# Performance work log

Hardware: AMD Instinct MI355X
Metric: run time of the kernel (lower is better)

## Reference

```python
import jax, jax.numpy as jnp
import numpy as np
import math

EMBED_DIM = 64

def setup_inputs() -> dict:
    key = jax.random.key(0)
    ks = jax.random.split(key, 9)
    B, S, H, E = 2, 2048, 8, EMBED_DIM
    f16 = jnp.float16
    inp = {
        'query': jax.random.normal(ks[0], (B, S, H, E), dtype=f16),
        'key':   jax.random.normal(ks[1], (B, S, H, E), dtype=f16),
        'value': jax.random.normal(ks[2], (B, S, H, E), dtype=f16),
        # Linear params (torch Linear: y = x @ W.T + b); W stored as [out,in]
        'Wq': (jax.random.normal(ks[3], (E, E), dtype=f16) / np.float16(math.sqrt(E))),
        'bq': jax.random.normal(ks[4], (E,), dtype=f16) * np.float16(0.02),
        'Wk': (jax.random.normal(ks[5], (E, E), dtype=f16) / np.float16(math.sqrt(E))),
        'bk': jax.random.normal(ks[6], (E,), dtype=f16) * np.float16(0.02),
        'Wv': (jax.random.normal(ks[7], (E, E), dtype=f16) / np.float16(math.sqrt(E))),
        'bv': jax.random.normal(ks[8], (E,), dtype=f16) * np.float16(0.02),
    }
    return inp

def reference(query, key, value, Wq, bq, Wk, bk, Wv, bv):
    # Linear projections on last dim, fused with permute(0,2,1,3): [B,S,H,E] -> [B,H,S,E]
    q = jnp.einsum('bshe,fe->bhsf', query, Wq) + bq
    k = jnp.einsum('bshe,fe->bhsf', key, Wk) + bk
    v = jnp.einsum('bshe,fe->bhsf', value, Wv) + bv
    scale = jnp.asarray(1.0 / math.sqrt(q.shape[-1]), dtype=q.dtype)
    q = q * scale
    # full attention matrix [B,H,S,S], fp16 matmul then fp32 softmax (faithful to source)
    scores = jnp.einsum('bhse,bhte->bhst', q, k).astype(jnp.float32)
    attn = jax.nn.softmax(scores, axis=-1).astype(jnp.float16)
    out = jnp.einsum('bhst,bhte->bhse', attn, v)
    return out
```

## Files before the change

### kernel.cpp

```cpp
#include <hip/hip_runtime.h>

#define S_LEN 2048
#define NH    8
#define EMB   64
#define BM    64
#define BN    64
#define NKT   (S_LEN / BN)
#define NSPLIT 2
#define M_INIT  (-1.0e4f)
#define EXP_CLAMP (-80.0f)
#define DEFER_THR 8.0f

typedef _Float16 half8   __attribute__((ext_vector_type(8)));
typedef _Float16 half4   __attribute__((ext_vector_type(4)));
typedef float    float4_t __attribute__((ext_vector_type(4)));
typedef float    float8_t __attribute__((ext_vector_type(8)));

__device__ inline half8 cvt8(const float* p) {
    float8_t f = *reinterpret_cast<const float8_t*>(p);
    half8 h;
    #pragma unroll
    for (int j = 0; j < 8; ++j) h[j] = (_Float16)f[j];
    return h;
}

__device__ inline void gload_lds16(const _Float16* g, _Float16* l) {
    __builtin_amdgcn_global_load_lds(
        (const __attribute__((address_space(1))) void*)g,
        (__attribute__((address_space(3))) void*)l, 16, 0, 0);
}

__device__ inline void proj_body(
    int mode, int bid, const float* __restrict__ X,
    const float* __restrict__ W, const float* __restrict__ bias,
    _Float16* __restrict__ Dst)
{
    const int tid  = threadIdx.x;
    const int lane = tid & 63;
    const int wave = tid >> 6;
    const int l15  = lane & 15;
    const int quad = lane >> 4;
    const int gwave = bid * 4 + wave;

    half8 wf[4][2];
    #pragma unroll
    for (int ft = 0; ft < 4; ++ft)
        #pragma unroll
        for (int ks = 0; ks < 2; ++ks)
            wf[ft][ks] = cvt8(W + (ft * 16 + l15) * 64 + ks * 32 + quad * 8);
    float bv[4];
    #pragma unroll
    for (int ft = 0; ft < 4; ++ft) bv[ft] = bias[ft * 16 + l15];

    #pragma unroll
    for (int rt2 = 0; rt2 < 2; ++rt2) {
        const int rt = gwave * 2 + rt2;
        const int arow = rt * 16 + l15;
        half8 xf[2];
        #pragma unroll
        for (int ks = 0; ks < 2; ++ks)
            xf[ks] = cvt8(X + (long)arow * 64 + ks * 32 + quad * 8);
        float4_t acc[4];
        #pragma unroll
        for (int ft = 0; ft < 4; ++ft) {
            acc[ft] = (float4_t){0.f, 0.f, 0.f, 0.f};
            #pragma unroll
            for (int ks = 0; ks < 2; ++ks)
                acc[ft] = __builtin_amdgcn_mfma_f32_16x16x32_f16(
                    xf[ks], wf[ft][ks], acc[ft], 0, 0, 0);
        }
        #pragma unroll
        for (int r = 0; r < 4; ++r) {
            const int row = rt * 16 + quad * 4 + r;
            const int b = row >> 14;
            const int s = (row >> 3) & 2047;
            const int h = row & 7;
            const int bh = b * NH + h;
            #pragma unroll
            for (int ft = 0; ft < 4; ++ft) {
                const _Float16 v = (_Float16)(acc[ft][r] + bv[ft]);
                const int f = ft * 16 + l15;
                if (mode == 0)
                    Dst[((long)bh * S_LEN + s) * EMB + f] = v * (_Float16)0.125f;
                else if (mode == 1)
                    Dst[(((long)bh * 8 + (f >> 3)) * S_LEN + s) * 8 + (f & 7)] = v;
                else
                    Dst[(((long)bh * 256 + (s >> 3)) * 64 + f) * 8 + (s & 7)] = v;
            }
        }
    }
}

__global__ __launch_bounds__(256) void proj_qkv(
    const float* __restrict__ q_in, const float* __restrict__ k_in,
    const float* __restrict__ v_in,
    const float* __restrict__ Wq, const float* __restrict__ bq,
    const float* __restrict__ Wk, const float* __restrict__ bk,
    const float* __restrict__ Wv, const float* __restrict__ bv_,
    _Float16* __restrict__ Qf16, _Float16* __restrict__ KT8,
    _Float16* __restrict__ VT8)
{
    const int seg = blockIdx.x >> 8;
    const int bid = blockIdx.x & 255;
    if (seg == 0)      proj_body(0, bid, q_in, Wq, bq, Qf16);
    else if (seg == 1) proj_body(1, bid, k_in, Wk, bk, KT8);
    else               proj_body(2, bid, v_in, Wv, bv_, VT8);
}

__global__ __launch_bounds__(256) void proj_qk(
    const float* __restrict__ q_in, const float* __restrict__ k_in,
    const float* __restrict__ Wq, const float* __restrict__ bq,
    const float* __restrict__ Wk, const float* __restrict__ bk,
    _Float16* __restrict__ Qf16, _Float16* __restrict__ KT8)
{
    const int seg = blockIdx.x >> 8;
    const int bid = blockIdx.x & 255;
    if (seg == 0) proj_body(0, bid, q_in, Wq, bq, Qf16);
    else          proj_body(1, bid, k_in, Wk, bk, KT8);
}

__global__ __launch_bounds__(256) void proj_v(
    const float* __restrict__ v_in,
    const float* __restrict__ Wv, const float* __restrict__ bv_,
    _Float16* __restrict__ VT8)
{
    proj_body(2, blockIdx.x, v_in, Wv, bv_, VT8);
}

__global__ __launch_bounds__(512, 4) void attn_fused(
    const _Float16* __restrict__ KT, const _Float16* __restrict__ VT,
    const _Float16* __restrict__ Qf16, float* __restrict__ out)
{
    extern __shared__ __align__(16) char smem[];
    _Float16* KV = (_Float16*)smem;

    const int tid  = threadIdx.x;
    const int lane = tid & 63;
    const int wave = tid >> 6;
    const int g    = wave >> 2;
    const int w4   = wave & 3;
    const int l15  = lane & 15;
    const int quad = lane >> 4;
    const int tid_g = tid & 255;

    _Float16* Kb0 = KV + (g * 4 + 0) * 4096;
    _Float16* Kb1 = KV + (g * 4 + 1) * 4096;
    _Float16* Vb0 = KV + (g * 4 + 2) * 4096;
    _Float16* Vb1 = KV + (g * 4 + 3) * 4096;
    _Float16* Pw  = (_Float16*)(smem + 65536) + wave * 1024;
    float*    mrgO  = (float*)(smem + 32768);
    float*    mrgML = (float*)(smem + 49152);

    const int bx  = blockIdx.x;
    const int xcd = bx & 7;
    const int j   = bx >> 3;
    const int hh  = j >> 5;
    const int qt  = j & 31;
    const int bh  = xcd * 2 + hh;

    const int qrow0 = qt * BM + w4 * 16;
    const _Float16* kg  = KT + (long)bh * 8 * S_LEN * 8;
    const _Float16* vgh = VT + (long)bh * 256 * 512;

    const _Float16* k0 = kg + ((long)(tid_g >> 6) * S_LEN + (tid_g & 63)) * 8;
    const _Float16* k1 = kg + ((long)((tid_g >> 6) + 4) * S_LEN + (tid_g & 63)) * 8;
    const _Float16* v0 = vgh + tid_g * 8;
    const _Float16* v1 = vgh + (256 + tid_g) * 8;

    const int kb = g * (NKT / NSPLIT);

    {
        const long t8  = (long)(kb * BN) * 8;
        const long t64 = (long)(kb * BN) * 64;
        gload_lds16(k0 + t8,  Kb0 + tid_g * 8);
        gload_lds16(k1 + t8,  Kb0 + (256 + tid_g) * 8);
        gload_lds16(v0 + t64, Vb0 + tid_g * 8);
        gload_lds16(v1 + t64, Vb0 + (256 + tid_g) * 8);
    }

    half8 qf[2];
    {
        const _Float16* qrow = Qf16 + ((long)bh * S_LEN + qrow0 + l15) * EMB;
        qf[0] = *reinterpret_cast<const half8*>(qrow + quad * 8);
        qf[1] = *reinterpret_cast<const half8*>(qrow + 32 + quad * 8);
    }

    half8 vones;
    #pragma unroll
    for (int jj = 0; jj < 8; ++jj) vones[jj] = (_Float16)1.0f;

    float4_t o[4];
    #pragma unroll
    for (int et = 0; et < 4; ++et) o[et] = (float4_t){0.f, 0.f, 0.f, 0.f};
    float4_t lacc = (float4_t){0.f, 0.f, 0.f, 0.f};
    float m_run = M_INIT;

    const int pswz = (l15 & 7) << 3;
    __syncthreads();

    for (int it = 0; it < NKT / NSPLIT; ++it) {
        const int cur = it & 1;
        const bool more = (it + 1 < NKT / NSPLIT);

        if (more) {
            const long t8  = (long)((kb + it + 1) * BN) * 8;
            const long t64 = (long)((kb + it + 1) * BN) * 64;
            _Float16* kd = cur ? Kb0 : Kb1;
            _Float16* vd = cur ? Vb0 : Vb1;
            gload_lds16(k0 + t8,  kd + tid_g * 8);
            gload_lds16(k1 + t8,  kd + (256 + tid_g) * 8);
            gload_lds16(v0 + t64, vd + tid_g * 8);
            gload_lds16(v1 + t64, vd + (256 + tid_g) * 8);
        }

        const _Float16* Kc = cur ? Kb1 : Kb0;
        const _Float16* Vc = cur ? Vb1 : Vb0;

        float4_t sacc[4];
        #pragma unroll
        for (int nt = 0; nt < 4; ++nt) sacc[nt] = (float4_t){0.f, 0.f, 0.f, 0.f};
        __builtin_amdgcn_s_setprio(1);
        #pragma unroll
        for (int nt = 0; nt < 4; ++nt)
            #pragma unroll
            for (int ks = 0; ks < 2; ++ks) {
                half8 kf = *reinterpret_cast<const half8*>(
                    Kc + (ks * 4 + quad) * 512 + (nt * 16 + l15) * 8);
                sacc[nt] = __builtin_amdgcn_mfma_f32_16x16x32_f16(
                    kf, qf[ks], sacc[nt], 0, 0, 0);
            }
        __builtin_amdgcn_s_setprio(0);

        float mx = fmaxf(fmaxf(sacc[0][0], sacc[0][1]),
                         fmaxf(sacc[0][2], sacc[0][3]));
        mx = fmaxf(fmaxf(mx, sacc[1][0]), sacc[1][1]);
        mx = fmaxf(fmaxf(mx, sacc[1][2]), sacc[1][3]);
        mx = fmaxf(fmaxf(mx, sacc[2][0]), sacc[2][1]);
        mx = fmaxf(fmaxf(mx, sacc[2][2]), sacc[2][3]);
        mx = fmaxf(fmaxf(mx, sacc[3][0]), sacc[3][1]);
        mx = fmaxf(fmaxf(mx, sacc[3][2]), sacc[3][3]);

        if (!__all(mx - m_run <= DEFER_THR)) {
            float mr = fmaxf(mx, __shfl_xor(mx, 16));
            mr = fmaxf(mr, __shfl_xor(mr, 32));
            const float mn = fmaxf(m_run, mr);
            const float alpha = __expf(fmaxf(m_run - mn, EXP_CLAMP));
            m_run = mn;
            #pragma unroll
            for (int r = 0; r < 4; ++r) {
                const float ar = __shfl(alpha, quad * 4 + r);
                lacc[r] *= ar;
                #pragma unroll
                for (int et = 0; et < 4; ++et) o[et][r] *= ar;
            }
        }

        #pragma unroll
        for (int nt = 0; nt < 4; ++nt) {
            half4 ph;
            #pragma unroll
            for (int r = 0; r < 4; ++r)
                ph[r] = (_Float16)__expf(sacc[nt][r] - m_run);
            *reinterpret_cast<half4*>(
                &Pw[l15 * 64 + ((nt * 16 + quad * 4) ^ pswz)]) = ph;
        }
        half8 pf0 = *reinterpret_cast<const half8*>(
            &Pw[l15 * 64 + ((quad * 8) ^ pswz)]);
        half8 pf1 = *reinterpret_cast<const half8*>(
            &Pw[l15 * 64 + ((32 + quad * 8) ^ pswz)]);

        __builtin_amdgcn_s_setprio(1);
        #pragma unroll
        for (int et = 0; et < 4; ++et) {
            half8 vf = *reinterpret_cast<const half8*>(
                Vc + quad * 512 + (et * 16 + l15) * 8);
            o[et] = __builtin_amdgcn_mfma_f32_16x16x32_f16(pf0, vf, o[et], 0, 0, 0);
        }
        lacc = __builtin_amdgcn_mfma_f32_16x16x32_f16(pf0, vones, lacc, 0, 0, 0);
        #pragma unroll
        for (int et = 0; et < 4; ++et) {
            half8 vf = *reinterpret_cast<const half8*>(
                Vc + (4 + quad) * 512 + (et * 16 + l15) * 8);
            o[et] = __builtin_amdgcn_mfma_f32_16x16x32_f16(pf1, vf, o[et], 0, 0, 0);
        }
        lacc = __builtin_amdgcn_mfma_f32_16x16x32_f16(pf1, vones, lacc, 0, 0, 0);
        __builtin_amdgcn_s_setprio(0);

        if (more) __syncthreads();
    }

    __syncthreads();
    if (g == 1) {
        float* mo = mrgO + w4 * 1024;
        #pragma unroll
        for (int r = 0; r < 4; ++r)
            #pragma unroll
            for (int et = 0; et < 4; ++et)
                mo[(quad * 4 + r) * 64 + et * 16 + l15] = o[et][r];
        if (lane < 16) mrgML[w4 * 32 + lane] = m_run;
        if (l15 == 0) {
            #pragma unroll
            for (int r = 0; r < 4; ++r)
                mrgML[w4 * 32 + 16 + quad * 4 + r] = lacc[r];
        }
    }
    __syncthreads();
    if (g == 0) {
        const float* mo = mrgO + w4 * 1024;
        #pragma unroll
        for (int r = 0; r < 4; ++r) {
            const int row = quad * 4 + r;
            const float m0r = __shfl(m_run, row);
            const float m1r = mrgML[w4 * 32 + row];
            const float l1r = mrgML[w4 * 32 + 16 + row];
            const float M = fmaxf(m0r, m1r);
            const float e0 = __expf(fmaxf(m0r - M, EXP_CLAMP));
            const float e1 = __expf(fmaxf(m1r - M, EXP_CLAMP));
            const float inv = 1.f / (lacc[r] * e0 + l1r * e1);
            const float w0 = e0 * inv, w1 = e1 * inv;
            const long orow = ((long)bh * S_LEN + qrow0 + row) * EMB;
            #pragma unroll
            for (int et = 0; et < 4; ++et) {
                const float val = o[et][r] * w0 +
                                  mo[row * 64 + et * 16 + l15] * w1;
                out[orow + et * 16 + l15] = (float)(_Float16)val;
            }
        }
    }
}

__global__ __launch_bounds__(256, 4) void attn_part(
    const _Float16* __restrict__ KT, const _Float16* __restrict__ VT,
    const _Float16* __restrict__ Qf16,
    _Float16* __restrict__ p0, _Float16* __restrict__ p1,
    float* __restrict__ stats)
{
    __shared__ __align__(16) _Float16 Kb[2][8 * 64 * 8];
    __shared__ __align__(16) _Float16 Vb[2][8 * 64 * 8];
    __shared__ __align__(16) _Float16 Pl[4][16 * 64];

    const int tid  = threadIdx.x;
    const int lane = tid & 63;
    const int wave = tid >> 6;
    const int l15  = lane & 15;
    const int quad = lane >> 4;

    const int bx     = blockIdx.x;
    const int xcd    = bx & 7;
    const int j      = bx >> 3;
    const int hh     = j >> 6;
    const int within = j & 63;
    const int bh     = xcd * 2 + hh;
    const int qt     = within >> 1;
    const int sp     = within & 1;

    const int qrow0 = qt * BM + wave * 16;
    const _Float16* kg  = KT + (long)bh * 8 * S_LEN * 8;
    const _Float16* vgh = VT + (long)bh * 256 * 512;

    const _Float16* k0 = kg + ((long)(tid >> 6) * S_LEN + (tid & 63)) * 8;
    const _Float16* k1 = kg + ((long)((tid >> 6) + 4) * S_LEN + (tid & 63)) * 8;
    const _Float16* v0 = vgh + tid * 8;
    const _Float16* v1 = vgh + (256 + tid) * 8;

    const int kb = sp * (NKT / NSPLIT), ke = kb + (NKT / NSPLIT);

    {
        const long t8  = (long)(kb * BN) * 8;
        const long t64 = (long)(kb * BN) * 64;
        gload_lds16(k0 + t8,  &Kb[0][tid * 8]);
        gload_lds16(k1 + t8,  &Kb[0][(256 + tid) * 8]);
        gload_lds16(v0 + t64, &Vb[0][tid * 8]);
        gload_lds16(v1 + t64, &Vb[0][(256 + tid) * 8]);
    }

    half8 qf[2];
    {
        const _Float16* qrow = Qf16 + ((long)bh * S_LEN + qrow0 + l15) * EMB;
        qf[0] = *reinterpret_cast<const half8*>(qrow + quad * 8);
        qf[1] = *reinterpret_cast<const half8*>(qrow + 32 + quad * 8);
    }

    half8 vones;
    #pragma unroll
    for (int jj = 0; jj < 8; ++jj) vones[jj] = (_Float16)1.0f;

    float4_t o[4];
    #pragma unroll
    for (int et = 0; et < 4; ++et) o[et] = (float4_t){0.f, 0.f, 0.f, 0.f};
    float4_t lacc = (float4_t){0.f, 0.f, 0.f, 0.f};
    float m_run = M_INIT;

    const int pswz = (l15 & 7) << 3;
    _Float16* Pw = Pl[wave];

    __syncthreads();

    for (int kt = kb; kt < ke; ++kt) {
        const int cur = (kt - kb) & 1;
        const bool more = (kt + 1 < ke);

        if (more) {
            const long t8  = (long)((kt + 1) * BN) * 8;
            const long t64 = (long)((kt + 1) * BN) * 64;
            _Float16* kd = Kb[cur ^ 1];
            _Float16* vd = Vb[cur ^ 1];
            gload_lds16(k0 + t8,  kd + tid * 8);
            gload_lds16(k1 + t8,  kd + (256 + tid) * 8);
            gload_lds16(v0 + t64, vd + tid * 8);
            gload_lds16(v1 + t64, vd + (256 + tid) * 8);
        }

        const _Float16* Kc = Kb[cur];
        const _Float16* Vc = Vb[cur];

        float4_t sacc[4];
        #pragma unroll
        for (int nt = 0; nt < 4; ++nt) sacc[nt] = (float4_t){0.f, 0.f, 0.f, 0.f};
        __builtin_amdgcn_s_setprio(1);
        #pragma unroll
        for (int nt = 0; nt < 4; ++nt)
            #pragma unroll
            for (int ks = 0; ks < 2; ++ks) {
                half8 kf = *reinterpret_cast<const half8*>(
                    Kc + (ks * 4 + quad) * 512 + (nt * 16 + l15) * 8);
                sacc[nt] = __builtin_amdgcn_mfma_f32_16x16x32_f16(
                    kf, qf[ks], sacc[nt], 0, 0, 0);
            }
        __builtin_amdgcn_s_setprio(0);

        float mx = fmaxf(fmaxf(sacc[0][0], sacc[0][1]),
                         fmaxf(sacc[0][2], sacc[0][3]));
        mx = fmaxf(fmaxf(mx, sacc[1][0]), sacc[1][1]);
        mx = fmaxf(fmaxf(mx, sacc[1][2]), sacc[1][3]);
        mx = fmaxf(fmaxf(mx, sacc[2][0]), sacc[2][1]);
        mx = fmaxf(fmaxf(mx, sacc[2][2]), sacc[2][3]);
        mx = fmaxf(fmaxf(mx, sacc[3][0]), sacc[3][1]);
        mx = fmaxf(fmaxf(mx, sacc[3][2]), sacc[3][3]);

        if (!__all(mx - m_run <= DEFER_THR)) {
            float mr = fmaxf(mx, __shfl_xor(mx, 16));
            mr = fmaxf(mr, __shfl_xor(mr, 32));
            const float mn = fmaxf(m_run, mr);
            const float alpha = __expf(fmaxf(m_run - mn, EXP_CLAMP));
            m_run = mn;
            #pragma unroll
            for (int r = 0; r < 4; ++r) {
                const float ar = __shfl(alpha, quad * 4 + r);
                lacc[r] *= ar;
                #pragma unroll
                for (int et = 0; et < 4; ++et) o[et][r] *= ar;
            }
        }

        #pragma unroll
        for (int nt = 0; nt < 4; ++nt) {
            half4 ph;
            #pragma unroll
            for (int r = 0; r < 4; ++r)
                ph[r] = (_Float16)__expf(sacc[nt][r] - m_run);
            *reinterpret_cast<half4*>(
                &Pw[l15 * 64 + ((nt * 16 + quad * 4) ^ pswz)]) = ph;
        }
        half8 pf0 = *reinterpret_cast<const half8*>(
            &Pw[l15 * 64 + ((quad * 8) ^ pswz)]);
        half8 pf1 = *reinterpret_cast<const half8*>(
            &Pw[l15 * 64 + ((32 + quad * 8) ^ pswz)]);

        __builtin_amdgcn_s_setprio(1);
        #pragma unroll
        for (int et = 0; et < 4; ++et) {
            half8 vf = *reinterpret_cast<const half8*>(
                Vc + quad * 512 + (et * 16 + l15) * 8);
            o[et] = __builtin_amdgcn_mfma_f32_16x16x32_f16(pf0, vf, o[et], 0, 0, 0);
        }
        lacc = __builtin_amdgcn_mfma_f32_16x16x32_f16(pf0, vones, lacc, 0, 0, 0);
        #pragma unroll
        for (int et = 0; et < 4; ++et) {
            half8 vf = *reinterpret_cast<const half8*>(
                Vc + (4 + quad) * 512 + (et * 16 + l15) * 8);
            o[et] = __builtin_amdgcn_mfma_f32_16x16x32_f16(pf1, vf, o[et], 0, 0, 0);
        }
        lacc = __builtin_amdgcn_mfma_f32_16x16x32_f16(pf1, vones, lacc, 0, 0, 0);
        __builtin_amdgcn_s_setprio(0);

        if (more) __syncthreads();
    }

    _Float16* pp = (sp == 0) ? p0 : p1;
    #pragma unroll
    for (int r = 0; r < 4; ++r) {
        const float inv = 1.f / lacc[r];
        const int row = qrow0 + quad * 4 + r;
        const int R = bh * S_LEN + row;
        #pragma unroll
        for (int et = 0; et < 4; ++et)
            pp[(long)R * EMB + et * 16 + l15] = (_Float16)(o[et][r] * inv);
    }
    {
        const int srcl = (lane >> 2) * 16;
        const float s0 = __shfl(lacc[0], srcl);
        const float s1 = __shfl(lacc[1], srcl);
        const float s2 = __shfl(lacc[2], srcl);
        const float s3 = __shfl(lacc[3], srcl);
        const int rr = lane & 3;
        const float lsel = (rr == 0) ? s0 : (rr == 1) ? s1 : (rr == 2) ? s2 : s3;
        if (lane < 16) {
            const int R = bh * S_LEN + qrow0 + lane;
            stats[sp * 32768 + R] = m_run;
            stats[(NSPLIT + sp) * 32768 + R] = lsel;
        }
    }
}

__global__ __launch_bounds__(256) void attn_combine(
    const _Float16* __restrict__ p0, const _Float16* __restrict__ p1,
    const float* __restrict__ stats, float* __restrict__ out)
{
    const int gid = blockIdx.x * 256 + threadIdx.x;
    const int R  = gid >> 2;
    const int c0 = (gid & 3) * 16;
    const float m0 = stats[R], m1 = stats[32768 + R];
    const float l0 = stats[2 * 32768 + R], l1 = stats[3 * 32768 + R];
    const float M = fmaxf(m0, m1);
    float w0 = l0 * __expf(fmaxf(m0 - M, EXP_CLAMP));
    float w1 = l1 * __expf(fmaxf(m1 - M, EXP_CLAMP));
    const float rinv = 1.f / (w0 + w1);
    w0 *= rinv; w1 *= rinv;
    const long i0 = (long)R * EMB + c0;
    #pragma unroll
    for (int h = 0; h < 2; ++h) {
        half8 a = *reinterpret_cast<const half8*>(p0 + i0 + h * 8);
        half8 b = *reinterpret_cast<const half8*>(p1 + i0 + h * 8);
        #pragma unroll
        for (int j = 0; j < 8; ++j)
            out[i0 + h * 8 + j] = (float)(_Float16)(
                w0 * (float)a[j] + w1 * (float)b[j]);
    }
}

extern "C" void kernel_launch(void* const* d_in, const int* in_sizes, int n_in,
                              void* d_out, int out_size, void* d_ws, size_t ws_size,
                              hipStream_t stream) {
    const float* q_in = (const float*)d_in[0];
    const float* k_in = (const float*)d_in[1];
    const float* v_in = (const float*)d_in[2];
    const float* Wq   = (const float*)d_in[3];
    const float* bq   = (const float*)d_in[4];
    const float* Wk   = (const float*)d_in[5];
    const float* bk   = (const float*)d_in[6];
    const float* Wv   = (const float*)d_in[7];
    const float* bv   = (const float*)d_in[8];
    float* out = (float*)d_out;

    if (ws_size >= (size_t)(12u << 20)) {
        _Float16* Qf16 = (_Float16*)d_ws;
        _Float16* KT8  = (_Float16*)((char*)d_ws + (4u << 20));
        _Float16* VT8  = (_Float16*)((char*)d_ws + (8u << 20));
        proj_qkv<<<768, 256, 0, stream>>>(q_in, k_in, v_in, Wq, bq, Wk, bk,
                                          Wv, bv, Qf16, KT8, VT8);
        attn_fused<<<512, 512, 81920, stream>>>(KT8, VT8, Qf16, out);
    } else {
        _Float16* Qf16  = (_Float16*)d_out;
        _Float16* KT8   = (_Float16*)((char*)d_out + (4u << 20));
        _Float16* part0 = (_Float16*)d_in[2];
        _Float16* part1 = part0 + (long)2 * 1024 * 1024;
        float*    stats = (float*)d_in[0];
        _Float16* VT8;
        if (ws_size >= (size_t)(4u << 20)) {
            VT8 = (_Float16*)d_ws;
            proj_qkv<<<768, 256, 0, stream>>>(q_in, k_in, v_in, Wq, bq, Wk, bk,
                                              Wv, bv, Qf16, KT8, VT8);
        } else {
            VT8 = (_Float16*)d_in[1];
            proj_qk<<<512, 256, 0, stream>>>(q_in, k_in, Wq, bq, Wk, bk,
                                             Qf16, KT8);
            proj_v<<<256, 256, 0, stream>>>(v_in, Wv, bv, VT8);
        }
        attn_part<<<16 * 32 * NSPLIT, 256, 0, stream>>>(KT8, VT8, Qf16,
                                                        part0, part1, stats);
        attn_combine<<<512, 256, 0, stream>>>(part0, part1, stats, out);
    }
}
```

Before: 121.1 us.

## Split KV loop across four wave groups per block with LDS merge

The fused attention kernel now uses 1024 threads, four groups of four waves, each handling a quarter of the key/value tiles instead of half. The partial outputs, maxima and sums of groups 1-3 are staged in LDS and merged by group 0 with a four-way rescale. This shortens each wave's serial KV loop and adds latency hiding inside a block. The cost is 160KB of dynamic LDS per block, which likely allows only one block per CU, plus a larger merge step.

Result: slower. 129.4 us (+6.9%).

```diff
diff --git a/kernel.cpp b/kernel.cpp
--- a/kernel.cpp
+++ b/kernel.cpp
@@ -7,6 +7,7 @@
 #define BN    64
 #define NKT   (S_LEN / BN)
 #define NSPLIT 2
+#define NG    4
 #define M_INIT  (-1.0e4f)
 #define EXP_CLAMP (-80.0f)
 #define DEFER_THR 8.0f
@@ -127,12 +128,11 @@
     proj_body(2, blockIdx.x, v_in, Wv, bv_, VT8);
 }
 
-__global__ __launch_bounds__(512, 4) void attn_fused(
+__global__ __launch_bounds__(1024, 4) void attn_fused4(
     const _Float16* __restrict__ KT, const _Float16* __restrict__ VT,
     const _Float16* __restrict__ Qf16, float* __restrict__ out)
 {
     extern __shared__ __align__(16) char smem[];
-    _Float16* KV = (_Float16*)smem;
 
     const int tid  = threadIdx.x;
     const int lane = tid & 63;
@@ -143,13 +143,11 @@
     const int quad = lane >> 4;
     const int tid_g = tid & 255;
 
-    _Float16* Kb0 = KV + (g * 4 + 0) * 4096;
-    _Float16* Kb1 = KV + (g * 4 + 1) * 4096;
-    _Float16* Vb0 = KV + (g * 4 + 2) * 4096;
-    _Float16* Vb1 = KV + (g * 4 + 3) * 4096;
-    _Float16* Pw  = (_Float16*)(smem + 65536) + wave * 1024;
-    float*    mrgO  = (float*)(smem + 32768);
-    float*    mrgML = (float*)(smem + 49152);
+    _Float16* Kb0 = (_Float16*)(smem + g * 32768);
+    _Float16* Kb1 = (_Float16*)(smem + g * 32768 + 8192);
+    _Float16* Vb0 = (_Float16*)(smem + g * 32768 + 16384);
+    _Float16* Vb1 = (_Float16*)(smem + g * 32768 + 24576);
+    _Float16* Pw  = (_Float16*)(smem + 131072 + wave * 2048);
 
     const int bx  = blockIdx.x;
     const int xcd = bx & 7;
@@ -167,7 +165,7 @@
     const _Float16* v0 = vgh + tid_g * 8;
     const _Float16* v1 = vgh + (256 + tid_g) * 8;
 
-    const int kb = g * (NKT / NSPLIT);
+    const int kb = g * (NKT / NG);
 
     {
         const long t8  = (long)(kb * BN) * 8;
@@ -198,9 +196,9 @@
     const int pswz = (l15 & 7) << 3;
     __syncthreads();
 
-    for (int it = 0; it < NKT / NSPLIT; ++it) {
+    for (int it = 0; it < NKT / NG; ++it) {
         const int cur = it & 1;
-        const bool more = (it + 1 < NKT / NSPLIT);
+        const bool more = (it + 1 < NKT / NG);
 
         if (more) {
             const long t8  = (long)((kb + it + 1) * BN) * 8;
@@ -290,40 +288,56 @@
     }
 
     __syncthreads();
-    if (g == 1) {
-        float* mo = mrgO + w4 * 1024;
+    if (g > 0) {
+        float* mo = (float*)(smem + g * 32768) + w4 * 1024;
         #pragma unroll
         for (int r = 0; r < 4; ++r)
             #pragma unroll
             for (int et = 0; et < 4; ++et)
                 mo[(quad * 4 + r) * 64 + et * 16 + l15] = o[et][r];
-        if (lane < 16) mrgML[w4 * 32 + lane] = m_run;
+        float* ml = (float*)(smem + g * 32768 + 16384) + w4 * 32;
+        if (lane < 16) ml[lane] = m_run;
         if (l15 == 0) {
             #pragma unroll
             for (int r = 0; r < 4; ++r)
-                mrgML[w4 * 32 + 16 + quad * 4 + r] = lacc[r];
+                ml[16 + quad * 4 + r] = lacc[r];
         }
     }
     __syncthreads();
+
     if (g == 0) {
-        const float* mo = mrgO + w4 * 1024;
         #pragma unroll
         for (int r = 0; r < 4; ++r) {
             const int row = quad * 4 + r;
             const float m0r = __shfl(m_run, row);
-            const float m1r = mrgML[w4 * 32 + row];
-            const float l1r = mrgML[w4 * 32 + 16 + row];
-            const float M = fmaxf(m0r, m1r);
+            float mg[3], lg[3];
+            #pragma unroll
+            for (int gg = 0; gg < 3; ++gg) {
+                const float* ml = (float*)(smem + (gg + 1) * 32768 + 16384)
+                                  + w4 * 32;
+                mg[gg] = ml[row];
+                lg[gg] = ml[16 + row];
+            }
+            float M = fmaxf(fmaxf(m0r, mg[0]), fmaxf(mg[1], mg[2]));
             const float e0 = __expf(fmaxf(m0r - M, EXP_CLAMP));
-            const float e1 = __expf(fmaxf(m1r - M, EXP_CLAMP));
-            const float inv = 1.f / (lacc[r] * e0 + l1r * e1);
-            const float w0 = e0 * inv, w1 = e1 * inv;
+            float e[3], denom = lacc[r] * e0;
+            #pragma unroll
+            for (int gg = 0; gg < 3; ++gg) {
+                e[gg] = __expf(fmaxf(mg[gg] - M, EXP_CLAMP));
+                denom += lg[gg] * e[gg];
+            }
+            const float inv = 1.f / denom;
             const long orow = ((long)bh * S_LEN + qrow0 + row) * EMB;
             #pragma unroll
             for (int et = 0; et < 4; ++et) {
-                const float val = o[et][r] * w0 +
-                                  mo[row * 64 + et * 16 + l15] * w1;
-                out[orow + et * 16 + l15] = (float)(_Float16)val;
+                float val = o[et][r] * e0;
+                #pragma unroll
+                for (int gg = 0; gg < 3; ++gg) {
+                    const float* mo = (float*)(smem + (gg + 1) * 32768)
+                                      + w4 * 1024;
+                    val += mo[row * 64 + et * 16 + l15] * e[gg];
+                }
+                out[orow + et * 16 + l15] = (float)(_Float16)(val * inv);
             }
         }
     }
@@ -557,9 +571,15 @@
         _Float16* Qf16 = (_Float16*)d_ws;
         _Float16* KT8  = (_Float16*)((char*)d_ws + (4u << 20));
         _Float16* VT8  = (_Float16*)((char*)d_ws + (8u << 20));
+        static bool attr_set = false;
+        if (!attr_set) {
+            (void)hipFuncSetAttribute((const void*)attn_fused4,
+                hipFuncAttributeMaxDynamicSharedMemorySize, 163840);
+            attr_set = true;
+        }
         proj_qkv<<<768, 256, 0, stream>>>(q_in, k_in, v_in, Wq, bq, Wk, bk,
                                           Wv, bv, Qf16, KT8, VT8);
-        attn_fused<<<512, 512, 81920, stream>>>(KT8, VT8, Qf16, out);
+        attn_fused4<<<512, 1024, 163840, stream>>>(KT8, VT8, Qf16, out);
     } else {
         _Float16* Qf16  = (_Float16*)d_out;
         _Float16* KT8   = (_Float16*)((char*)d_out + (4u << 20));
```
